# Performance work log

Hardware: AMD Instinct MI355X
Metric: run time of the kernel (lower is better)

The kernel has to match this reference:

```python
import jax, jax.numpy as jnp
import numpy as np

B = 512      # batch
T = 16       # tokens per instruction
V = 1000     # vocab
E = 4        # num_experts
K = 1        # active experts per layer
NLAYERS = 3
TOPK_LOGIC = 32


def _conv(x, w, b, stride=2):
    # x: [B,Cin,H,W], w: [Cout,Cin,3,3] (OIHW), padding=1, stride=2
    y = jax.lax.conv_general_dilated(
        x, w, window_strides=(stride, stride), padding=((1, 1), (1, 1)),
        dimension_numbers=('NCHW', 'OIHW', 'NCHW'))
    return y + b[None, :, None, None]


def _gated_conv(x, w, b, gate):
    # w: [E,Cout,Cin,3,3], b: [E,Cout], gate: [B,E] 0/1 mask
    # Faithful to original: all experts computed densely, then masked.
    outs = jax.vmap(lambda wi, bi: _conv(x, wi, bi))(w, b)  # [E,B,Cout,H',W']
    return jnp.einsum('ebchw,be->bchw', outs, gate)


def _topk_mask(logits, k):
    # 0/1 mask with ones at the top-k positions along the last axis
    _, idx = jax.lax.top_k(logits, k)
    return jnp.sum(jax.nn.one_hot(idx, logits.shape[-1], dtype=logits.dtype), axis=-2)


def setup_inputs() -> dict:
    key = jax.random.key(0)
    ks = jax.random.split(key, 16)
    def rn(k, shape, s=0.05):
        return jax.random.normal(k, shape, jnp.float32) * s
    return dict(
        img=jax.random.normal(ks[0], (B, 12, 56, 56), jnp.float32),
        text=jax.random.randint(ks[1], (B, T), 0, V),
        prev_action=jax.random.randint(ks[2], (B,), 0, 7),
        emb_table=rn(ks[3], (V, 32), 1.0),
        r_w1=rn(ks[4], (32, 64)), r_b1=jnp.zeros((64,), jnp.float32),
        r_w2=rn(ks[5], (64, NLAYERS * E)), r_b2=jnp.zeros((NLAYERS * E,), jnp.float32),
        l_w1=rn(ks[6], (32, 64)), l_b1=jnp.zeros((64,), jnp.float32),
        l_w2=rn(ks[7], (64, 256)), l_b2=jnp.zeros((256,), jnp.float32),
        c1_w=rn(ks[8], (E, 32, 12, 3, 3)), c1_b=jnp.zeros((E, 32), jnp.float32),
        c2_w=rn(ks[9], (E, 64, 32, 3, 3)), c2_b=jnp.zeros((E, 64), jnp.float32),
        c3_w=rn(ks[10], (E, 128, 64, 3, 3)), c3_b=jnp.zeros((E, 128), jnp.float32),
        act_emb=rn(ks[11], (7, 16), 1.0),
        f_w=rn(ks[12], (6272 + 32 + 16, 256)), f_b=jnp.zeros((256,), jnp.float32),
        h_w=rn(ks[13], (256, 5)), h_b=jnp.zeros((5,), jnp.float32),
    )


def reference(img, text, prev_action, emb_table, r_w1, r_b1, r_w2, r_b2,
              l_w1, l_b1, l_w2, l_b2, c1_w, c1_b, c2_w, c2_b, c3_w, c3_b,
              act_emb, f_w, f_b, h_w, h_b):
    # EmbeddingBag(mode='mean') over token dim
    lang = jnp.mean(emb_table[text], axis=1)                      # [B,32]
    # Router: MLP -> [B,3,E] logits, top-k scatter -> 0/1 mask
    rlog = (jax.nn.relu(lang @ r_w1 + r_b1) @ r_w2 + r_b2).reshape(-1, NLAYERS, E)
    masks = _topk_mask(rlog, K)                                   # [B,3,E]
    x = jax.nn.relu(_gated_conv(img, c1_w, c1_b, masks[:, 0, :])) # [B,32,28,28]
    x = jax.nn.relu(_gated_conv(x, c2_w, c2_b, masks[:, 1, :]))   # [B,64,14,14]
    x = jax.nn.relu(_gated_conv(x, c3_w, c3_b, masks[:, 2, :]))   # [B,128,7,7]
    vis = x.reshape(x.shape[0], -1)                               # [B,6272]
    act = act_emb[prev_action]                                    # [B,16]
    fused = jnp.concatenate([vis, lang, act], axis=1)             # [B,6320]
    hidden = fused @ f_w + f_b                                    # [B,256]
    logic = jax.nn.relu(lang @ l_w1 + l_b1) @ l_w2 + l_b2         # [B,256]
    lmask = _topk_mask(logic, TOPK_LOGIC)                         # [B,256]
    out = jax.nn.relu(hidden * lmask)                             # dropout is identity in eval
    logits = out @ h_w + h_b                                      # [B,5]
    return logits, rlog
```

## Files before the change

kernel.cpp:

```cpp
#include <hip/hip_runtime.h>
#include <hip/hip_bf16.h>


typedef __bf16 bf16x8 __attribute__((ext_vector_type(8)));
typedef float f32x4 __attribute__((ext_vector_type(4)));

__device__ __forceinline__ unsigned short f2bf(float f) {
  union { float f; unsigned u; } v; v.f = f;
  unsigned r = v.u + 0x7FFFu + ((v.u >> 16) & 1u);
  return (unsigned short)(r >> 16);
}

__global__ __launch_bounds__(256) void prep_kernel(
    const float* __restrict__ img,
    const int* __restrict__ text, const float* __restrict__ emb,
    const float* __restrict__ r_w1, const float* __restrict__ r_b1,
    const float* __restrict__ r_w2, const float* __restrict__ r_b2,
    const float* __restrict__ l_w1, const float* __restrict__ l_b1,
    const float* __restrict__ l_w2, const float* __restrict__ l_b2,
    const float* __restrict__ act_emb, const int* __restrict__ pa,
    const float* __restrict__ c1_w, const float* __restrict__ c2_w,
    const float* __restrict__ c3_w, const float* __restrict__ fw,
    float* __restrict__ rlog_out, int* __restrict__ eidx, float* __restrict__ lmask,
    unsigned short* __restrict__ tailb,
    unsigned short* __restrict__ x0b,
    unsigned short* __restrict__ wb1, unsigned short* __restrict__ wb2,
    unsigned short* __restrict__ wb3, unsigned short* __restrict__ fwT) {
  __shared__ __align__(16) char shm[64 * 72 * 2];
  const int blk = blockIdx.x;
  const int tid = threadIdx.x;

  if (blk < 512) {
    int b = blk;
    int t = tid;
    __shared__ float lg[32];
    __shared__ float hr[64];
    __shared__ float hl[64];
    __shared__ float rl[12];
    __shared__ float lgc[256];

    if (t < 32) {
      const int* tb = text + b * 16;
      float s = 0.f;
#pragma unroll
      for (int tok = 0; tok < 16; ++tok) s += emb[tb[tok] * 32 + t];
      lg[t] = s * 0.0625f;
    }
    __syncthreads();

    if (t < 64) {
      float s1 = r_b1[t], s2 = l_b1[t];
      for (int k = 0; k < 32; ++k) {
        float lv = lg[k];
        s1 += lv * r_w1[k * 64 + t];
        s2 += lv * l_w1[k * 64 + t];
      }
      hr[t] = fmaxf(s1, 0.f);
      hl[t] = fmaxf(s2, 0.f);
    }
    if (t < 64) {
      float v = 0.f;
      if (t < 32) v = lg[t];
      else if (t < 48) v = act_emb[pa[b] * 16 + (t - 32)];
      tailb[b * 64 + t] = f2bf(v);
    }
    __syncthreads();

    if (t < 12) {
      float s = r_b2[t];
      for (int k = 0; k < 64; ++k) s += hr[k] * r_w2[k * 12 + t];
      rl[t] = s;
      rlog_out[b * 12 + t] = s;
    }
    {
      float s = l_b2[t];
      for (int k = 0; k < 64; ++k) s += hl[k] * l_w2[k * 256 + t];
      lgc[t] = s;
    }
    __syncthreads();

    if (t < 3) {
      int best = 0;
      float bv = rl[t * 4];
      for (int e = 1; e < 4; ++e) {
        float v = rl[t * 4 + e];
        if (v > bv) { bv = v; best = e; }
      }
      eidx[b * 3 + t] = best;
    }
    {
      float v = lgc[t];
      int cnt = 0;
      for (int k = 0; k < 256; ++k) {
        float u = lgc[k];
        cnt += (u > v) || (u == v && k < t);
      }
      lmask[b * 256 + t] = (cnt < 32) ? 1.f : 0.f;
    }
  } else if (blk < 2080) {
    int idx = (blk - 512) * 256 + tid;
    if (idx < 24576) {
      int k = idx % 192, ec = idx / 192;
      float v = 0.f;
      if (k < 144) {
        int g = k >> 4, ci = k & 15;
        if (ci < 12) v = c1_w[ec * 108 + ci * 9 + g];
      }
      wb1[idx] = f2bf(v);
    } else if (idx < 106496) {
      int i2 = idx - 24576;
      int k = i2 % 320, ec = i2 / 320;
      float v = 0.f;
      if (k < 288) {
        int g = k >> 5, ci = k & 31;
        v = c2_w[ec * 288 + ci * 9 + g];
      }
      wb2[i2] = f2bf(v);
    } else {
      int i3 = idx - 106496;
      int k = i3 % 576, ec = i3 / 576;
      int g = k >> 6, ci = k & 63;
      wb3[i3] = f2bf(c3_w[ec * 576 + ci * 9 + g]);
    }
  } else if (blk < 2476) {
    unsigned short(*tl)[72] = (unsigned short(*)[72])shm;
    int fb = blk - 2080;
    int kblk = fb >> 2, nblk = fb & 3;
    int n0 = nblk * 64;
    int k0 = kblk * 64;
    int rl = tid >> 2;
    int c4 = (tid & 3) * 16;
    int srow;
    bool valid;
    if (kblk < 98) {
      int p = kblk >> 1;
      int c0 = (kblk & 1) * 64;
      srow = (c0 + rl) * 49 + p;
      valid = true;
    } else {
      srow = 6272 + rl;
      valid = (rl < 48);
    }
#pragma unroll
    for (int h = 0; h < 4; ++h) {
      float4 v = valid ? *(const float4*)&fw[(size_t)srow * 256 + n0 + c4 + h * 4]
                       : (float4){0.f, 0.f, 0.f, 0.f};
      tl[rl][c4 + h * 4 + 0] = f2bf(v.x);
      tl[rl][c4 + h * 4 + 1] = f2bf(v.y);
      tl[rl][c4 + h * 4 + 2] = f2bf(v.z);
      tl[rl][c4 + h * 4 + 3] = f2bf(v.w);
    }
    __syncthreads();
    int nloc = tid >> 2;
    int kc = (tid & 3) * 16;
    unsigned short vv[16];
#pragma unroll
    for (int i = 0; i < 16; ++i) vv[i] = tl[kc + i][nloc];
    unsigned short* dst = fwT + (size_t)(n0 + nloc) * 6336 + k0 + kc;
    *(uint4*)dst = *(const uint4*)&vv[0];
    *(uint4*)(dst + 8) = *(const uint4*)&vv[8];
  } else {
    int idx4 = (blk - 2476) * 256 + tid;
    int s = idx4 / 784;
    int q = idx4 - s * 784;
    const float* ib = img + (size_t)s * 37632 + q * 4;
    float4 v[12];
#pragma unroll
    for (int ci = 0; ci < 12; ++ci) v[ci] = *(const float4*)&ib[ci * 3136];
    unsigned short o16[64];
#pragma unroll
    for (int j = 0; j < 4; ++j) {
      o16[j * 16 + 0]  = f2bf(j == 0 ? v[0].x : j == 1 ? v[0].y : j == 2 ? v[0].z : v[0].w);
#pragma unroll
      for (int ci = 1; ci < 12; ++ci) {
        float fv = (j == 0) ? v[ci].x : (j == 1) ? v[ci].y : (j == 2) ? v[ci].z : v[ci].w;
        o16[j * 16 + ci] = f2bf(fv);
      }
#pragma unroll
      for (int ci = 12; ci < 16; ++ci) o16[j * 16 + ci] = 0;
    }
    uint4* dst = (uint4*)(x0b + (size_t)idx4 * 64);
#pragma unroll
    for (int h = 0; h < 8; ++h) dst[h] = *(const uint4*)&o16[h * 8];
  }
}

__global__ __launch_bounds__(256) void bucket_kernel(const int* __restrict__ eidx,
                                                     int* __restrict__ cnt,
                                                     int* __restrict__ perm) {
  int l = blockIdx.x;
  __shared__ int el[512];
  __shared__ int cc[4];
  int t = threadIdx.x;
  el[t] = eidx[t * 3 + l];
  el[t + 256] = eidx[(t + 256) * 3 + l];
  __syncthreads();
  if (t < 4) {
    int c = 0;
    for (int b = 0; b < 512; ++b) c += (el[b] == t);
    cc[t] = c;
    cnt[l * 4 + t] = c;
  }
  __syncthreads();
#pragma unroll
  for (int rep = 0; rep < 2; ++rep) {
    int b = t + rep * 256;
    int e = el[b];
    int rank = 0;
    for (int bp = 0; bp < b; ++bp) rank += (el[bp] == e);
    int off = 0;
    for (int ee = 0; ee < e; ++ee) off += cc[ee];
    perm[l * 512 + off + rank] = b;
  }
}

template<int CIN, int H, int OH, int KREAL, int KP, int COUT,
         int WGM, int WGN, int MF, int NF>
__global__ __launch_bounds__(256) void conv_mfma(
    const unsigned short* __restrict__ in, const unsigned short* __restrict__ wb,
    const float* __restrict__ bias, const int* __restrict__ cnt,
    const int* __restrict__ perm, unsigned short* __restrict__ out) {
  constexpr int PerS = OH * OH;
  constexpr int BM = WGM * MF * 16;
  constexpr int BN = WGN * NF * 16;
  constexpr int AJ = BM / 32;
  constexpr int KT = KP / 64;
  constexpr int W = H;
  constexpr int BCH = BN / 32;

  int bm = blockIdx.x;
  int e = 0, row0 = 0, rows = 0;
  bool found = false;
  {
    int acc = 0, ebase = 0;
#pragma unroll
    for (int ee = 0; ee < 4; ++ee) {
      int er = cnt[ee] * PerS;
      int te = (er + BM - 1) / BM;
      if (!found && bm < acc + te) {
        e = ee;
        row0 = ebase + (bm - acc) * BM;
        rows = er - (bm - acc) * BM;
        if (rows > BM) rows = BM;
        found = true;
      }
      acc += te;
      ebase += er;
    }
  }
  if (!found) return;

  __shared__ __align__(16) char lds[BM * 128 + BN * 128];
  char* ldsB = lds + BM * 128;
  const int tid = threadIdx.x;
  const int lane = tid & 63;
  const int wid = tid >> 6;
  const int wm0 = (wid / WGN) * (MF * 16);
  const int wn0 = (wid % WGN) * (NF * 16);
  const int c16 = tid & 7;

  int ihc[AJ], iwc[AJ], abase[AJ], adso[AJ];
#pragma unroll
  for (int j = 0; j < AJ; ++j) {
    int r = (tid >> 3) + 32 * j;
    int gr = row0 + r;
    const int MAXR = 512 * PerS - 1;
    if (gr > MAXR) gr = MAXR;
    int sord = gr / PerS;
    int p = gr - sord * PerS;
    int s = perm[sord];
    int oh = p / OH, ow = p - oh * OH;
    ihc[j] = oh * 2 - 1;
    iwc[j] = ow * 2 - 1;
    abase[j] = s * (H * W);
    adso[j] = r * 128 + ((c16 * 16) ^ ((r & 7) << 4));
  }
  const unsigned short* wbe = wb + (size_t)e * COUT * KP;
  int bgo[BCH], bdso[BCH];
#pragma unroll
  for (int c = 0; c < BCH; ++c) {
    int cc = tid + 256 * c;
    int n = cc >> 3, cb = cc & 7;
    bgo[c] = n * KP + cb * 8;
    bdso[c] = n * 128 + ((cb * 16) ^ ((n & 7) << 4));
  }
  int ardo[MF], arx[MF], brdo[NF], brx[NF];
#pragma unroll
  for (int mf = 0; mf < MF; ++mf) {
    int r = wm0 + mf * 16 + (lane & 15);
    ardo[mf] = r * 128;
    arx[mf] = (r & 7) << 4;
  }
#pragma unroll
  for (int nf = 0; nf < NF; ++nf) {
    int n = wn0 + nf * 16 + (lane & 15);
    brdo[nf] = n * 128;
    brx[nf] = (n & 7) << 4;
  }

  auto loadA = [&](int kt, int j) -> uint4 {
    uint4 z; z.x = z.y = z.z = z.w = 0u;
    int kbase = kt * 64 + c16 * 8;
    if (kbase >= KREAL) return z;
    int g = kbase / CIN;
    int ci0 = kbase - g * CIN;
    int kh = g / 3, kw = g - (g / 3) * 3;
    int ih = ihc[j] + kh, iw = iwc[j] + kw;
    if ((unsigned)ih >= (unsigned)H || (unsigned)iw >= (unsigned)W) return z;
    const unsigned short* p = in + ((size_t)(abase[j] + ih * W + iw) * CIN + ci0);
    return *(const uint4*)p;
  };

  uint4 rA[AJ], rB[BCH];
#pragma unroll
  for (int j = 0; j < AJ; ++j) rA[j] = loadA(0, j);
#pragma unroll
  for (int c = 0; c < BCH; ++c) rB[c] = *(const uint4*)(wbe + bgo[c]);

  f32x4 acc[MF][NF];
#pragma unroll
  for (int mf = 0; mf < MF; ++mf)
#pragma unroll
    for (int nf = 0; nf < NF; ++nf) acc[mf][nf] = (f32x4){0.f, 0.f, 0.f, 0.f};

  for (int kt = 0; kt < KT; ++kt) {
    __syncthreads();
#pragma unroll
    for (int j = 0; j < AJ; ++j) *(uint4*)(lds + adso[j]) = rA[j];
#pragma unroll
    for (int c = 0; c < BCH; ++c) *(uint4*)(ldsB + bdso[c]) = rB[c];
    __syncthreads();
    if (kt + 1 < KT) {
#pragma unroll
      for (int j = 0; j < AJ; ++j) rA[j] = loadA(kt + 1, j);
#pragma unroll
      for (int c = 0; c < BCH; ++c) rB[c] = *(const uint4*)(wbe + bgo[c] + (kt + 1) * 64);
    }
#pragma unroll
    for (int ks = 0; ks < 2; ++ks) {
      int cb = ks * 64 + ((lane >> 4) << 4);
      bf16x8 af[MF], bfv[NF];
#pragma unroll
      for (int mf = 0; mf < MF; ++mf)
        af[mf] = __builtin_bit_cast(bf16x8, *(const uint4*)(lds + ardo[mf] + (cb ^ arx[mf])));
#pragma unroll
      for (int nf = 0; nf < NF; ++nf)
        bfv[nf] = __builtin_bit_cast(bf16x8, *(const uint4*)(ldsB + brdo[nf] + (cb ^ brx[nf])));
#pragma unroll
      for (int mf = 0; mf < MF; ++mf)
#pragma unroll
        for (int nf = 0; nf < NF; ++nf)
          acc[mf][nf] = __builtin_amdgcn_mfma_f32_16x16x32_bf16(af[mf], bfv[nf], acc[mf][nf], 0, 0, 0);
    }
  }

  const int col = lane & 15;
  const int rg = (lane >> 4) * 4;
#pragma unroll
  for (int mf = 0; mf < MF; ++mf) {
#pragma unroll
    for (int r = 0; r < 4; ++r) {
      int m = wm0 + mf * 16 + rg + r;
      if (m < rows) {
        int gr = row0 + m;
        int sord = gr / PerS;
        int p = gr - sord * PerS;
        int s = perm[sord];
        size_t ob = ((size_t)s * PerS + p) * COUT;
#pragma unroll
        for (int nf = 0; nf < NF; ++nf) {
          int co = wn0 + nf * 16 + col;
          float v = acc[mf][nf][r] + bias[e * COUT + co];
          out[ob + co] = f2bf(fmaxf(v, 0.f));
        }
      }
    }
  }
}

__global__ __launch_bounds__(256) void fgemm_kernel(
    const unsigned short* __restrict__ x3, const unsigned short* __restrict__ tail,
    const unsigned short* __restrict__ fwT, float* __restrict__ partial) {
  constexpr int MF = 2, NF = 2;
  const int row0 = blockIdx.x * 64;
  const int nc0 = blockIdx.y * 64;
  const int kz = blockIdx.z * 704;
  __shared__ __align__(16) char lds[64 * 128 + 64 * 128];
  char* ldsB = lds + 64 * 128;
  const int tid = threadIdx.x;
  const int lane = tid & 63;
  const int wid = tid >> 6;
  const int wm0 = (wid >> 1) * 32;
  const int wn0 = (wid & 1) * 32;
  const int c16 = tid & 7;
  int arow[2], adso[2];
#pragma unroll
  for (int j = 0; j < 2; ++j) {
    int r = (tid >> 3) + 32 * j;
    arow[j] = row0 + r;
    adso[j] = r * 128 + ((c16 * 16) ^ ((r & 7) << 4));
  }
  int bgo[2], bdso[2];
#pragma unroll
  for (int c = 0; c < 2; ++c) {
    int cc = tid + 256 * c;
    int n = cc >> 3, cb = cc & 7;
    bgo[c] = (nc0 + n) * 6336 + kz + cb * 8;
    bdso[c] = n * 128 + ((cb * 16) ^ ((n & 7) << 4));
  }
  int ardo[MF], arx[MF], brdo[NF], brx[NF];
#pragma unroll
  for (int mf = 0; mf < MF; ++mf) {
    int r = wm0 + mf * 16 + (lane & 15);
    ardo[mf] = r * 128; arx[mf] = (r & 7) << 4;
  }
#pragma unroll
  for (int nf = 0; nf < NF; ++nf) {
    int n = wn0 + nf * 16 + (lane & 15);
    brdo[nf] = n * 128; brx[nf] = (n & 7) << 4;
  }
  auto loadA = [&](int kt, int j) -> uint4 {
    int k = kz + kt * 64 + c16 * 8;
    const unsigned short* p;
    if (k < 6272) p = x3 + (size_t)arow[j] * 6272 + k;
    else p = tail + arow[j] * 64 + (k - 6272);
    return *(const uint4*)p;
  };
  uint4 rA[2], rB[2];
#pragma unroll
  for (int j = 0; j < 2; ++j) rA[j] = loadA(0, j);
#pragma unroll
  for (int c = 0; c < 2; ++c) rB[c] = *(const uint4*)(fwT + bgo[c]);
  f32x4 acc[MF][NF];
#pragma unroll
  for (int mf = 0; mf < MF; ++mf)
#pragma unroll
    for (int nf = 0; nf < NF; ++nf) acc[mf][nf] = (f32x4){0.f, 0.f, 0.f, 0.f};

  for (int kt = 0; kt < 11; ++kt) {
    __syncthreads();
#pragma unroll
    for (int j = 0; j < 2; ++j) *(uint4*)(lds + adso[j]) = rA[j];
#pragma unroll
    for (int c = 0; c < 2; ++c) *(uint4*)(ldsB + bdso[c]) = rB[c];
    __syncthreads();
    if (kt + 1 < 11) {
#pragma unroll
      for (int j = 0; j < 2; ++j) rA[j] = loadA(kt + 1, j);
#pragma unroll
      for (int c = 0; c < 2; ++c) rB[c] = *(const uint4*)(fwT + bgo[c] + (kt + 1) * 64);
    }
#pragma unroll
    for (int ks = 0; ks < 2; ++ks) {
      int cb = ks * 64 + ((lane >> 4) << 4);
      bf16x8 af[MF], bfv[NF];
#pragma unroll
      for (int mf = 0; mf < MF; ++mf)
        af[mf] = __builtin_bit_cast(bf16x8, *(const uint4*)(lds + ardo[mf] + (cb ^ arx[mf])));
#pragma unroll
      for (int nf = 0; nf < NF; ++nf)
        bfv[nf] = __builtin_bit_cast(bf16x8, *(const uint4*)(ldsB + brdo[nf] + (cb ^ brx[nf])));
#pragma unroll
      for (int mf = 0; mf < MF; ++mf)
#pragma unroll
        for (int nf = 0; nf < NF; ++nf)
          acc[mf][nf] = __builtin_amdgcn_mfma_f32_16x16x32_bf16(af[mf], bfv[nf], acc[mf][nf], 0, 0, 0);
    }
  }
  const int col = lane & 15;
  const int rg = (lane >> 4) * 4;
  float* pz = partial + (size_t)blockIdx.z * 131072;
#pragma unroll
  for (int mf = 0; mf < MF; ++mf)
#pragma unroll
    for (int r = 0; r < 4; ++r) {
      int m = wm0 + mf * 16 + rg + r;
      int grow = row0 + m;
#pragma unroll
      for (int nf = 0; nf < NF; ++nf) {
        int n = nc0 + wn0 + nf * 16 + col;
        pz[grow * 256 + n] = acc[mf][nf][r];
      }
    }
}

__global__ __launch_bounds__(256) void reduce_head(const float* __restrict__ part,
                                                   const float* __restrict__ f_b,
                                                   const float* __restrict__ lmask,
                                                   const float* __restrict__ h_w,
                                                   const float* __restrict__ h_b,
                                                   float* __restrict__ logits) {
  int b = blockIdx.x, t = threadIdx.x;
  float s = f_b[t];
#pragma unroll
  for (int z = 0; z < 9; ++z) s += part[z * 131072 + b * 256 + t];
  __shared__ float o[256];
  o[t] = (lmask[b * 256 + t] != 0.f) ? fmaxf(s, 0.f) : 0.f;
  __syncthreads();
  if (t < 5) {
    float v = h_b[t];
    for (int n = 0; n < 256; ++n) v += o[n] * h_w[n * 5 + t];
    logits[b * 5 + t] = v;
  }
}

extern "C" void kernel_launch(void* const* d_in, const int* in_sizes, int n_in,
                              void* d_out, int out_size, void* d_ws, size_t ws_size,
                              hipStream_t stream) {
  (void)in_sizes; (void)n_in; (void)out_size; (void)ws_size;
  const float* img       = (const float*)d_in[0];
  const int*   text      = (const int*)d_in[1];
  const int*   pa        = (const int*)d_in[2];
  const float* emb_table = (const float*)d_in[3];
  const float* r_w1 = (const float*)d_in[4];
  const float* r_b1 = (const float*)d_in[5];
  const float* r_w2 = (const float*)d_in[6];
  const float* r_b2 = (const float*)d_in[7];
  const float* l_w1 = (const float*)d_in[8];
  const float* l_b1 = (const float*)d_in[9];
  const float* l_w2 = (const float*)d_in[10];
  const float* l_b2 = (const float*)d_in[11];
  const float* c1_w = (const float*)d_in[12];
  const float* c1_b = (const float*)d_in[13];
  const float* c2_w = (const float*)d_in[14];
  const float* c2_b = (const float*)d_in[15];
  const float* c3_w = (const float*)d_in[16];
  const float* c3_b = (const float*)d_in[17];
  const float* act_emb = (const float*)d_in[18];
  const float* f_w = (const float*)d_in[19];
  const float* f_b = (const float*)d_in[20];
  const float* h_w = (const float*)d_in[21];
  const float* h_b = (const float*)d_in[22];

  float* outf   = (float*)d_out;
  float* logits = outf;
  float* rlog   = outf + 2560;

  char* cur = (char*)d_ws;
  auto alloc = [&](size_t bytes) { char* r = cur; cur += (bytes + 255) & ~(size_t)255; return r; };
  float* lmask   = (float*)alloc(131072 * 4);
  int* eidx      = (int*)alloc(1536 * 4);
  int* cnt       = (int*)alloc(12 * 4);
  int* perm      = (int*)alloc(1536 * 4);
  unsigned short* wb1  = (unsigned short*)alloc((size_t)24576 * 2);
  unsigned short* wb2  = (unsigned short*)alloc((size_t)81920 * 2);
  unsigned short* wb3  = (unsigned short*)alloc((size_t)294912 * 2);
  unsigned short* fwT  = (unsigned short*)alloc((size_t)1622016 * 2);
  unsigned short* tailb= (unsigned short*)alloc((size_t)32768 * 2);
  unsigned short* x1b  = (unsigned short*)alloc((size_t)12845056 * 2);
  unsigned short* x0b  = (unsigned short*)alloc((size_t)25690112 * 2);
  unsigned short* x2b  = x0b;
  unsigned short* x3b  = x0b + 6422528;
  float* partial       = (float*)(x0b + 6422528 + 3211264);

  prep_kernel<<<4044, 256, 0, stream>>>(img, text, emb_table,
                                        r_w1, r_b1, r_w2, r_b2,
                                        l_w1, l_b1, l_w2, l_b2,
                                        act_emb, pa,
                                        c1_w, c2_w, c3_w, f_w,
                                        rlog, eidx, lmask, tailb,
                                        x0b, wb1, wb2, wb3, fwT);
  bucket_kernel<<<3, 256, 0, stream>>>(eidx, cnt, perm);

  conv_mfma<16, 56, 28, 144, 192, 32, 4, 1, 2, 2>
      <<<3139, 256, 0, stream>>>(x0b, wb1, c1_b, cnt + 0, perm + 0, x1b);
  conv_mfma<32, 28, 14, 288, 320, 64, 2, 2, 4, 2>
      <<<787, 256, 0, stream>>>(x1b, wb2, c2_b, cnt + 4, perm + 512, x2b);
  conv_mfma<64, 14, 7, 576, 576, 128, 1, 4, 4, 2>
      <<<395, 256, 0, stream>>>(x2b, wb3, c3_b, cnt + 8, perm + 1024, x3b);

  fgemm_kernel<<<dim3(8, 4, 9), 256, 0, stream>>>(x3b, tailb, fwT, partial);
  reduce_head<<<512, 256, 0, stream>>>(partial, f_b, lmask, h_w, h_b, logits);
}
```

Before: 156.3 us.

## Fuse image fp32-to-bf16 conversion into a dedicated per-sample conv1 kernel

```diff
diff --git a/kernel.cpp b/kernel.cpp
--- a/kernel.cpp
+++ b/kernel.cpp
@@ -4,6 +4,7 @@
 
 typedef __bf16 bf16x8 __attribute__((ext_vector_type(8)));
 typedef float f32x4 __attribute__((ext_vector_type(4)));
+typedef unsigned short u16x8 __attribute__((ext_vector_type(8)));
 
 __device__ __forceinline__ unsigned short f2bf(float f) {
   union { float f; unsigned u; } v; v.f = f;
@@ -12,7 +13,6 @@
 }
 
 __global__ __launch_bounds__(256) void prep_kernel(
-    const float* __restrict__ img,
     const int* __restrict__ text, const float* __restrict__ emb,
     const float* __restrict__ r_w1, const float* __restrict__ r_b1,
     const float* __restrict__ r_w2, const float* __restrict__ r_b2,
@@ -23,7 +23,6 @@
     const float* __restrict__ c3_w, const float* __restrict__ fw,
     float* __restrict__ rlog_out, int* __restrict__ eidx, float* __restrict__ lmask,
     unsigned short* __restrict__ tailb,
-    unsigned short* __restrict__ x0b,
     unsigned short* __restrict__ wb1, unsigned short* __restrict__ wb2,
     unsigned short* __restrict__ wb3, unsigned short* __restrict__ fwT) {
   __shared__ __align__(16) char shm[64 * 72 * 2];
@@ -122,7 +121,7 @@
       int g = k >> 6, ci = k & 63;
       wb3[i3] = f2bf(c3_w[ec * 576 + ci * 9 + g]);
     }
-  } else if (blk < 2476) {
+  } else {
     unsigned short(*tl)[72] = (unsigned short(*)[72])shm;
     int fb = blk - 2080;
     int kblk = fb >> 2, nblk = fb & 3;
@@ -159,29 +158,6 @@
     unsigned short* dst = fwT + (size_t)(n0 + nloc) * 6336 + k0 + kc;
     *(uint4*)dst = *(const uint4*)&vv[0];
     *(uint4*)(dst + 8) = *(const uint4*)&vv[8];
-  } else {
-    int idx4 = (blk - 2476) * 256 + tid;
-    int s = idx4 / 784;
-    int q = idx4 - s * 784;
-    const float* ib = img + (size_t)s * 37632 + q * 4;
-    float4 v[12];
-#pragma unroll
-    for (int ci = 0; ci < 12; ++ci) v[ci] = *(const float4*)&ib[ci * 3136];
-    unsigned short o16[64];
-#pragma unroll
-    for (int j = 0; j < 4; ++j) {
-      o16[j * 16 + 0]  = f2bf(j == 0 ? v[0].x : j == 1 ? v[0].y : j == 2 ? v[0].z : v[0].w);
-#pragma unroll
-      for (int ci = 1; ci < 12; ++ci) {
-        float fv = (j == 0) ? v[ci].x : (j == 1) ? v[ci].y : (j == 2) ? v[ci].z : v[ci].w;
-        o16[j * 16 + ci] = f2bf(fv);
-      }
-#pragma unroll
-      for (int ci = 12; ci < 16; ++ci) o16[j * 16 + ci] = 0;
-    }
-    uint4* dst = (uint4*)(x0b + (size_t)idx4 * 64);
-#pragma unroll
-    for (int h = 0; h < 8; ++h) dst[h] = *(const uint4*)&o16[h * 8];
   }
 }
 
@@ -212,6 +188,138 @@
     for (int ee = 0; ee < e; ++ee) off += cc[ee];
     perm[l * 512 + off + rank] = b;
   }
+}
+
+__global__ __launch_bounds__(256) void conv1_fused(
+    const float* __restrict__ img, const unsigned short* __restrict__ wb,
+    const float* __restrict__ bias, const int* __restrict__ eidx,
+    unsigned short* __restrict__ out) {
+  const int s = blockIdx.x / 7;
+  const int t = blockIdx.x % 7;
+  const int e = eidx[s * 3];
+  __shared__ __align__(16) unsigned short lds_in[12288];
+  __shared__ __align__(16) char ldsB[3 * 4096];
+  const int tid = threadIdx.x;
+  const int lane = tid & 63;
+  const int wid = tid >> 6;
+  const int wm0 = wid * 32;
+
+  const int p0 = t * 128;
+  const int ohmin = p0 / 28;
+  const int ih0 = ohmin * 2 - 1;
+
+  {
+    uint4 z; z.x = z.y = z.z = z.w = 0u;
+    uint4* q = (uint4*)lds_in;
+#pragma unroll
+    for (int i = 0; i < 6; ++i) q[tid + 256 * i] = z;
+  }
+  __syncthreads();
+
+  for (int task = tid; task < 312; task += 256) {
+    int row = task >> 1, half = task & 1;
+    int ci = row / 13, ihl = row - ci * 13;
+    int ih = ih0 + ihl;
+    if ((unsigned)ih < 56u) {
+      const float* src = img + (size_t)s * 37632 + ci * 3136 + ih * 56 + half * 28;
+      unsigned short* dst = lds_in + ci * 728 + ihl * 56 + half * 28;
+#pragma unroll
+      for (int u = 0; u < 7; ++u) {
+        float4 v = *(const float4*)(src + u * 4);
+        unsigned short w4[4] = {f2bf(v.x), f2bf(v.y), f2bf(v.z), f2bf(v.w)};
+        *(unsigned long long*)(dst + u * 4) = *(const unsigned long long*)w4;
+      }
+    }
+  }
+  {
+    const unsigned short* wbe = wb + e * (32 * 192);
+#pragma unroll
+    for (int c = 0; c < 3; ++c) {
+      int cc = tid + 256 * c;
+      int n = cc / 24, cb = cc - n * 24;
+      int kt = cb >> 3, cbl = cb & 7;
+      uint4 v = *(const uint4*)(wbe + n * 192 + cb * 8);
+      *(uint4*)(ldsB + kt * 4096 + n * 128 + ((cbl * 16) ^ ((n & 7) << 4))) = v;
+    }
+  }
+
+  int ohr[2], owr[2];
+#pragma unroll
+  for (int mf = 0; mf < 2; ++mf) {
+    int m = wm0 + mf * 16 + (lane & 15);
+    int p = p0 + m;
+    if (p > 783) p = 783;
+    ohr[mf] = p / 28;
+    owr[mf] = p - ohr[mf] * 28;
+  }
+  const int lg = lane >> 4;
+  const int ci0 = (lg & 1) * 8;
+  const int lgh = lg >> 1;
+  int brdo[2], brx[2];
+#pragma unroll
+  for (int nf = 0; nf < 2; ++nf) {
+    int n = nf * 16 + (lane & 15);
+    brdo[nf] = n * 128;
+    brx[nf] = (n & 7) << 4;
+  }
+
+  f32x4 acc[2][2];
+#pragma unroll
+  for (int mf = 0; mf < 2; ++mf)
+#pragma unroll
+    for (int nf = 0; nf < 2; ++nf) acc[mf][nf] = (f32x4){0.f, 0.f, 0.f, 0.f};
+
+  __syncthreads();
+
+#pragma unroll
+  for (int kt = 0; kt < 3; ++kt) {
+#pragma unroll
+    for (int ks = 0; ks < 2; ++ks) {
+      const int g = kt * 4 + ks * 2 + lgh;
+      const int kh = g / 3;
+      const int kw = g - kh * 3;
+      bf16x8 af[2];
+#pragma unroll
+      for (int mf = 0; mf < 2; ++mf) {
+        int iw = owr[mf] * 2 - 1 + kw;
+        int ihl = (ohr[mf] - ohmin) * 2 + kh;
+        bool valid = (g < 9) && (iw >= 0);
+        const unsigned short* bp = lds_in + ci0 * 728 + ihl * 56 + iw;
+        u16x8 a;
+#pragma unroll
+        for (int j = 0; j < 8; ++j) a[j] = valid ? bp[j * 728] : (unsigned short)0;
+        af[mf] = __builtin_bit_cast(bf16x8, a);
+      }
+      bf16x8 bfv[2];
+      const int cb = ks * 64 + ((lane >> 4) << 4);
+#pragma unroll
+      for (int nf = 0; nf < 2; ++nf)
+        bfv[nf] = __builtin_bit_cast(bf16x8,
+            *(const uint4*)(ldsB + kt * 4096 + brdo[nf] + (cb ^ brx[nf])));
+#pragma unroll
+      for (int mf = 0; mf < 2; ++mf)
+#pragma unroll
+        for (int nf = 0; nf < 2; ++nf)
+          acc[mf][nf] = __builtin_amdgcn_mfma_f32_16x16x32_bf16(af[mf], bfv[nf], acc[mf][nf], 0, 0, 0);
+    }
+  }
+
+  const int col = lane & 15;
+  const int rg = (lane >> 4) * 4;
+  const float b0 = bias[e * 32 + col];
+  const float b1 = bias[e * 32 + 16 + col];
+#pragma unroll
+  for (int mf = 0; mf < 2; ++mf)
+#pragma unroll
+    for (int r = 0; r < 4; ++r) {
+      int m = wm0 + mf * 16 + rg + r;
+      int p = p0 + m;
+      if (p < 784) {
+        size_t ob = ((size_t)s * 784 + p) * 32;
+        out[ob + col]      = f2bf(fmaxf(acc[mf][0][r] + b0, 0.f));
+        out[ob + 16 + col] = f2bf(fmaxf(acc[mf][1][r] + b1, 0.f));
+      }
+    }
 }
 
 template<int CIN, int H, int OH, int KREAL, int KP, int COUT,
@@ -548,22 +656,20 @@
   unsigned short* fwT  = (unsigned short*)alloc((size_t)1622016 * 2);
   unsigned short* tailb= (unsigned short*)alloc((size_t)32768 * 2);
   unsigned short* x1b  = (unsigned short*)alloc((size_t)12845056 * 2);
-  unsigned short* x0b  = (unsigned short*)alloc((size_t)25690112 * 2);
-  unsigned short* x2b  = x0b;
-  unsigned short* x3b  = x0b + 6422528;
-  float* partial       = (float*)(x0b + 6422528 + 3211264);
-
-  prep_kernel<<<4044, 256, 0, stream>>>(img, text, emb_table,
+  unsigned short* x2b  = (unsigned short*)alloc((size_t)6422528 * 2);
+  unsigned short* x3b  = (unsigned short*)alloc((size_t)3211264 * 2);
+  float* partial       = (float*)alloc((size_t)9 * 131072 * 4);
+
+  prep_kernel<<<2476, 256, 0, stream>>>(text, emb_table,
                                         r_w1, r_b1, r_w2, r_b2,
                                         l_w1, l_b1, l_w2, l_b2,
                                         act_emb, pa,
                                         c1_w, c2_w, c3_w, f_w,
                                         rlog, eidx, lmask, tailb,
-                                        x0b, wb1, wb2, wb3, fwT);
+                                        wb1, wb2, wb3, fwT);
   bucket_kernel<<<3, 256, 0, stream>>>(eidx, cnt, perm);
 
-  conv_mfma<16, 56, 28, 144, 192, 32, 4, 1, 2, 2>
-      <<<3139, 256, 0, stream>>>(x0b, wb1, c1_b, cnt + 0, perm + 0, x1b);
+  conv1_fused<<<3584, 256, 0, stream>>>(img, wb1, c1_b, eidx, x1b);
   conv_mfma<32, 28, 14, 288, 320, 64, 2, 2, 4, 2>
       <<<787, 256, 0, stream>>>(x1b, wb2, c2_b, cnt + 4, perm + 512, x2b);
   conv_mfma<64, 14, 7, 576, 576, 128, 1, 4, 4, 2>
```

New measurement: 151.2 us. 3.2% less time.
